# Optimization experiments

Hardware: AMD Instinct MI355X
Metric: run time of the kernel (lower is better)

Reference implementation:

```python
import jax, jax.numpy as jnp
import numpy as np

K = 1024
T = 16384
P = 2          # number of lags
N_STAGES = 2   # len(s_list)
EDGE_P = 0.005 # edge density -> avg degree ~5


def setup_inputs() -> dict:
    key = jax.random.key(0)
    kX, kA, ka, kb0, kb1 = jax.random.split(key, 5)
    X = jax.random.normal(kX, (K, T), dtype=jnp.float32)
    # sparse symmetric 0/1 adjacency, zero diagonal
    U = jax.random.uniform(kA, (K, K))
    Ab = (U < EDGE_P)
    Ab = (Ab | Ab.T) & ~jnp.eye(K, dtype=bool)
    A = Ab.astype(jnp.float32)
    alpha = jax.random.normal(ka, (P,), dtype=jnp.float32)
    beta0 = jax.random.normal(kb0, (P,), dtype=jnp.float32)
    beta1 = jax.random.normal(kb1, (P,), dtype=jnp.float32)
    return {"X": X, "A": A, "alpha": alpha, "beta0": beta0, "beta1": beta1}


def _stage_avg_matrices(A):
    """M[r] averages over nodes at shortest-path distance exactly r+1 (rows with
    no stage-r neighbors are all-zero, matching the `if neighbors:` guard)."""
    Ab = A > 0.5
    Af = Ab.astype(jnp.float32)
    reach_prev = jnp.eye(A.shape[0], dtype=bool)  # distance <= 0
    Ms = []
    for _ in range(N_STAGES):
        reach = reach_prev | ((reach_prev.astype(jnp.float32) @ Af) > 0.5)
        exact = reach & ~reach_prev                     # distance == r+1
        exact_f = exact.astype(jnp.float32)
        deg = exact_f.sum(axis=1, keepdims=True)        # (K, 1)
        M = exact_f / jnp.maximum(deg, 1.0)             # zero rows stay zero
        Ms.append(M)
        reach_prev = reach
    return Ms


def reference(X, A, alpha, beta0, beta1):
    K_, T_ = X.shape
    betas = [beta0, beta1]
    Ms = _stage_avg_matrices(A)
    # one dense aggregation per stage over ALL time steps, then slice lags
    MXs = [M @ X for M in Ms]                           # each (K, T)
    Y = jnp.zeros((K_, T_ - P), dtype=X.dtype)
    for lag in range(1, P + 1):
        sl = slice(P - lag, T_ - lag)
        Y = Y + alpha[lag - 1] * X[:, sl]
        for stage in range(N_STAGES):
            Y = Y + betas[stage][lag - 1] * MXs[stage][:, sl]
    return Y
```

## Files before the change

### kernel.cpp

```cpp
#include <hip/hip_runtime.h>

typedef float fx4 __attribute__((ext_vector_type(4)));
typedef short s16x8 __attribute__((ext_vector_type(8)));
typedef __bf16 bfx8 __attribute__((ext_vector_type(8)));

#define KN 1024
#define TT 16384
#define NOUT 16382
#define NKT 32

#define APK_OFF 67108864u

__device__ __forceinline__ unsigned short f2bf(float f) {
  return __builtin_bit_cast(unsigned short, (__bf16)f);
}

__device__ __forceinline__ void gll16(const void* g, void* l) {
  __builtin_amdgcn_global_load_lds(
      (const __attribute__((address_space(1))) void*)g,
      (__attribute__((address_space(3))) void*)l, 16, 0, 0);
}

__global__ __launch_bounds__(256) void k_masks(const float* __restrict__ A,
                                               unsigned* __restrict__ B1) {
  int k = blockIdx.x;
  int tid = threadIdx.x;
  int wv = tid >> 6, lane = tid & 63;
  for (int i = 0; i < 4; ++i) {
    int n = i * 256 + wv * 64 + lane;
    bool bit = (A[(size_t)k * KN + n] > 0.5f) && (n != k);
    unsigned long long m = __ballot(bit);
    if (lane == 0) {
      B1[k * 32 + i * 8 + wv * 2]     = (unsigned)m;
      B1[k * 32 + i * 8 + wv * 2 + 1] = (unsigned)(m >> 32);
    }
  }
}

__global__ __launch_bounds__(256) void k_weights(const unsigned* __restrict__ B1,
                                                 const float* __restrict__ alpha,
                                                 const float* __restrict__ beta0,
                                                 const float* __restrict__ beta1,
                                                 unsigned short* __restrict__ Wc) {
  __shared__ unsigned reach[32];
  __shared__ unsigned ex2[32];
  __shared__ unsigned short list[1056];
  __shared__ int nl;
  int k = blockIdx.x, tid = threadIdx.x;
  if (tid == 0) nl = 0;
  if (tid < 32) {
    unsigned r = B1[k * 32 + tid];
    if (tid == (k >> 5)) r |= 1u << (k & 31);
    reach[tid] = r;
    ex2[tid] = 0;
  }
  __syncthreads();
  for (int m = tid; m < KN; m += 256)
    if ((reach[m >> 5] >> (m & 31)) & 1) {
      int i = atomicAdd(&nl, 1);
      list[i] = (unsigned short)m;
    }
  __syncthreads();
  int n2 = nl;
  for (int i = 0; i < n2; ++i) {
    int m = list[i];
    if (tid < 32) ex2[tid] |= B1[m * 32 + tid];
  }
  __syncthreads();
  if (tid < 32) ex2[tid] &= ~reach[tid];
  __syncthreads();
  int d1 = 0, d2 = 0;
  for (int w = 0; w < 32; ++w) { d1 += __popc(reach[w]); d2 += __popc(ex2[w]); }
  d1 -= 1;
  float rd1 = 1.0f / fmaxf((float)d1, 1.0f);
  float rd2 = 1.0f / fmaxf((float)d2, 1.0f);
  float c00 = beta0[0] * rd1, c01 = beta0[1] * rd1;
  float c10 = beta1[0] * rd2, c11 = beta1[1] * rd2;
  float a0 = alpha[0], a1 = alpha[1];
  int mb = k >> 8, rloc = k & 255;
  for (int q = 0; q < 4; ++q) {
    int n = tid * 4 + q;
    bool in1 = (((reach[n >> 5] >> (n & 31)) & 1) != 0) && (n != k);
    bool in2 = ((ex2[n >> 5] >> (n & 31)) & 1) != 0;
    float v0 = (in1 ? c00 : 0.f) + (in2 ? c10 : 0.f) + (n == k ? a0 : 0.f);
    float v1 = (in1 ? c01 : 0.f) + (in2 ? c11 : 0.f) + (n == k ? a1 : 0.f);
    int kt = n >> 5, qk = (n >> 4) & 1, kb = (n >> 2) & 3, ii = (n & 3) * 2;
    size_t idx = ((((size_t)(mb * 32 + kt) * 2 + qk) * 4 + kb) * 256 + rloc) * 8 + ii;
    unsigned pair = (unsigned)f2bf(v0) | ((unsigned)f2bf(v1) << 16);
    *reinterpret_cast<unsigned*>(Wc + idx) = pair;
  }
}

__global__ __launch_bounds__(256) void k_pack_x2(const float* __restrict__ X,
                                                 unsigned short* __restrict__ Bpk) {
  int G = blockIdx.x * 256 + threadIdx.x;
  int col = G & 255;
  int kb  = (G >> 8) & 3;
  int qk  = (G >> 10) & 1;
  int kt  = (G >> 11) & 31;
  int jb  = G >> 16;
  int j   = jb * 256 + col;
  int mbase = kt * 32 + qk * 16 + kb * 4;
  unsigned v[4];
#pragma unroll
  for (int p = 0; p < 4; ++p) {
    int m = mbase + p;
    int j1 = j + 1;
    float f0 = (j1 < TT) ? X[(size_t)m * TT + j1] : 0.0f;
    float f1 = X[(size_t)m * TT + j];
    v[p] = (unsigned)f2bf(f0) | ((unsigned)f2bf(f1) << 16);
  }
  uint4 w; w.x = v[0]; w.y = v[1]; w.z = v[2]; w.w = v[3];
  *reinterpret_cast<uint4*>(Bpk + (size_t)G * 8) = w;
}

__global__ __launch_bounds__(512, 2) void k_gemm(const char* __restrict__ Apk,
                                                 const char* __restrict__ Bpk,
                                                 float* __restrict__ Y) {
  __shared__ char lds[131072];
  int bid = blockIdx.x;
  int swz = (bid & 7) * 32 + (bid >> 3);
  int jb = swz >> 2, mb = swz & 3;
  int tid = threadIdx.x;
  int lane = tid & 63, wv = tid >> 6;
  int wm = wv >> 2, wn = wv & 3;
  int kb = lane >> 4, ml = lane & 15;
  const char* Asrc = Apk + (size_t)mb * (NKT * 2 * 16384);
  const char* Bsrc = Bpk + (size_t)jb * (NKT * 2 * 16384);

  fx4 acc[2][4][4];
#pragma unroll
  for (int q = 0; q < 2; ++q)
#pragma unroll
    for (int a = 0; a < 4; ++a)
#pragma unroll
      for (int b = 0; b < 4; ++b) acc[q][a][b] = (fx4){0.f, 0.f, 0.f, 0.f};

  auto stage_half = [&](int tile, int isB, int qh) {
    char* dst = lds + (tile & 1) * 65536 + isB * 32768 + qh * 16384;
    const char* src = (isB ? Bsrc : Asrc) + ((size_t)(tile & (NKT - 1)) * 2 + qh) * 16384;
    gll16(src + tid * 16, dst + tid * 16);
    gll16(src + (size_t)(tid + 512) * 16, dst + (tid + 512) * 16);
  };

#define READ_A(dst, t, qk, qm)                                                      \
  do {                                                                              \
    const char* Ah_ = lds + ((t) & 1) * 65536 + (qk) * 16384;                       \
    _Pragma("unroll") for (int mf = 0; mf < 4; ++mf)                                \
      dst[mf] = *(const s16x8*)(Ah_ +                                               \
          (size_t)(kb * 256 + wm * 128 + (qm) * 64 + mf * 16 + ml) * 16);           \
  } while (0)
#define READ_B(dst, t, qk)                                                          \
  do {                                                                              \
    const char* Bh_ = lds + ((t) & 1) * 65536 + 32768 + (qk) * 16384;               \
    _Pragma("unroll") for (int nf = 0; nf < 4; ++nf)                                \
      dst[nf] = *(const s16x8*)(Bh_ +                                               \
          (size_t)(kb * 256 + wn * 64 + nf * 16 + ml) * 16);                        \
  } while (0)
#define MFMA16(acc_, a_, b_)                                                        \
  do {                                                                              \
    __builtin_amdgcn_s_setprio(1);                                                  \
    _Pragma("unroll") for (int mf = 0; mf < 4; ++mf)                                \
      _Pragma("unroll") for (int nf = 0; nf < 4; ++nf)                              \
        acc_[mf][nf] = __builtin_amdgcn_mfma_f32_16x16x32_bf16(                     \
            __builtin_bit_cast(bfx8, a_[mf]), __builtin_bit_cast(bfx8, b_[nf]),     \
            acc_[mf][nf], 0, 0, 0);                                                 \
    __builtin_amdgcn_s_setprio(0);                                                  \
  } while (0)

  s16x8 aA[4], aB[4], bA[4], bB[4];

  stage_half(0, 0, 0); stage_half(0, 1, 0);
  stage_half(0, 0, 1); stage_half(0, 1, 1);
  stage_half(1, 0, 0); stage_half(1, 1, 0);
  asm volatile("s_waitcnt vmcnt(4)" ::: "memory");
  __builtin_amdgcn_s_barrier();
  READ_A(aA, 0, 0, 0);
  READ_B(bA, 0, 0);

  for (int kt = 0; kt < NKT; ++kt) {
    READ_A(aB, kt, 0, 1);
    stage_half(kt + 1, 0, 1);
    MFMA16(acc[0], aA, bA);
    READ_A(aA, kt, 1, 0);
    READ_B(bB, kt, 1);
    stage_half(kt + 1, 1, 1);
    MFMA16(acc[1], aB, bA);
    asm volatile("s_waitcnt vmcnt(4)" ::: "memory");
    __builtin_amdgcn_s_barrier();
    READ_A(aB, kt, 1, 1);
    stage_half(kt + 2, 0, 0);
    MFMA16(acc[0], aA, bB);
    READ_A(aA, kt + 1, 0, 0);
    READ_B(bA, kt + 1, 0);
    stage_half(kt + 2, 1, 0);
    MFMA16(acc[1], aB, bB);
    asm volatile("s_waitcnt vmcnt(4)" ::: "memory");
    __builtin_amdgcn_s_barrier();
  }
  asm volatile("s_waitcnt vmcnt(0)" ::: "memory");

  int c0 = jb * 256 + wn * 64;
  int r0 = mb * 256 + wm * 128;
#pragma unroll
  for (int qm = 0; qm < 2; ++qm)
#pragma unroll
    for (int mf = 0; mf < 4; ++mf)
#pragma unroll
      for (int nf = 0; nf < 4; ++nf) {
        int c = c0 + nf * 16 + ml;
        if (c < NOUT) {
          int r = r0 + qm * 64 + mf * 16 + (lane >> 4) * 4;
#pragma unroll
          for (int i = 0; i < 4; ++i)
            Y[(size_t)(r + i) * NOUT + c] = acc[qm][mf][nf][i];
        }
      }
#undef READ_A
#undef READ_B
#undef MFMA16
}

extern "C" void kernel_launch(void* const* d_in, const int* in_sizes, int n_in,
                              void* d_out, int out_size, void* d_ws, size_t ws_size,
                              hipStream_t stream) {
  const float* X     = (const float*)d_in[0];
  const float* A     = (const float*)d_in[1];
  const float* alpha = (const float*)d_in[2];
  const float* beta0 = (const float*)d_in[3];
  const float* beta1 = (const float*)d_in[4];
  float* Y = (float*)d_out;
  char* ws = (char*)d_ws;
  char* Bpk = ws;
  char* Apk = ws + APK_OFF;
  unsigned* B1 = (unsigned*)ws;

  k_masks<<<dim3(1024), dim3(256), 0, stream>>>(A, B1);
  k_weights<<<dim3(1024), dim3(256), 0, stream>>>(B1, alpha, beta0, beta1,
                                                  (unsigned short*)Apk);
  k_pack_x2<<<dim3(16384), dim3(256), 0, stream>>>(X, (unsigned short*)Bpk);
  k_gemm<<<dim3(256), dim3(512), 0, stream>>>(Apk, Bpk, Y);
}
```

Measured before the change: 94.23 us.

## Switch GEMM to 32x32x16 bf16 MFMA with matching operand packing layout

Replaces the 16x16x32 MFMA tiling with 32x32x16 bf16 MFMA instructions, so each wave computes 4x2 fragments of 32x32 instead of 2x4x4 of 16x16. The packing kernels for both the weight matrix and the lagged X operand are rewritten to a new K-slice/octet layout that matches the 32x32 operand fragment format, and the LDS read and epilogue store indexing are updated to match. The larger MFMA reduces LDS fragment reads per FLOP and instruction issue overhead, at the cost of different register pressure and a strided epilogue write pattern.

```diff
diff --git a/kernel.cpp b/kernel.cpp
--- a/kernel.cpp
+++ b/kernel.cpp
@@ -1,6 +1,6 @@
 #include <hip/hip_runtime.h>
 
-typedef float fx4 __attribute__((ext_vector_type(4)));
+typedef float f32x16 __attribute__((ext_vector_type(16)));
 typedef short s16x8 __attribute__((ext_vector_type(8)));
 typedef __bf16 bfx8 __attribute__((ext_vector_type(8)));
 
@@ -84,8 +84,9 @@
     bool in2 = ((ex2[n >> 5] >> (n & 31)) & 1) != 0;
     float v0 = (in1 ? c00 : 0.f) + (in2 ? c10 : 0.f) + (n == k ? a0 : 0.f);
     float v1 = (in1 ? c01 : 0.f) + (in2 ? c11 : 0.f) + (n == k ? a1 : 0.f);
-    int kt = n >> 5, qk = (n >> 4) & 1, kb = (n >> 2) & 3, ii = (n & 3) * 2;
-    size_t idx = ((((size_t)(mb * 32 + kt) * 2 + qk) * 4 + kb) * 256 + rloc) * 8 + ii;
+    int kt = n >> 5, ks = (n >> 3) & 3, koct = (n >> 2) & 1, ii = (n & 3) * 2;
+    size_t idx = ((size_t)(mb * 32 + kt)) * 16384 + ks * 4096 + koct * 2048 +
+                 rloc * 8 + ii;
     unsigned pair = (unsigned)f2bf(v0) | ((unsigned)f2bf(v1) << 16);
     *reinterpret_cast<unsigned*>(Wc + idx) = pair;
   }
@@ -94,13 +95,13 @@
 __global__ __launch_bounds__(256) void k_pack_x2(const float* __restrict__ X,
                                                  unsigned short* __restrict__ Bpk) {
   int G = blockIdx.x * 256 + threadIdx.x;
-  int col = G & 255;
-  int kb  = (G >> 8) & 3;
-  int qk  = (G >> 10) & 1;
-  int kt  = (G >> 11) & 31;
-  int jb  = G >> 16;
-  int j   = jb * 256 + col;
-  int mbase = kt * 32 + qk * 16 + kb * 4;
+  int col  = G & 255;
+  int koct = (G >> 8) & 1;
+  int ks   = (G >> 9) & 3;
+  int kt   = (G >> 11) & 31;
+  int jb   = G >> 16;
+  int j    = jb * 256 + col;
+  int mbase = kt * 32 + ks * 8 + koct * 4;
   unsigned v[4];
 #pragma unroll
   for (int p = 0; p < 4; ++p) {
@@ -124,17 +125,19 @@
   int tid = threadIdx.x;
   int lane = tid & 63, wv = tid >> 6;
   int wm = wv >> 2, wn = wv & 3;
-  int kb = lane >> 4, ml = lane & 15;
-  const char* Asrc = Apk + (size_t)mb * (NKT * 2 * 16384);
-  const char* Bsrc = Bpk + (size_t)jb * (NKT * 2 * 16384);
-
-  fx4 acc[2][4][4];
-#pragma unroll
-  for (int q = 0; q < 2; ++q)
-#pragma unroll
-    for (int a = 0; a < 4; ++a)
-#pragma unroll
-      for (int b = 0; b < 4; ++b) acc[q][a][b] = (fx4){0.f, 0.f, 0.f, 0.f};
+  int l31 = lane & 31, loct = lane >> 5;
+  const char* Asrc = Apk + (size_t)mb * (NKT * 32768);
+  const char* Bsrc = Bpk + (size_t)jb * (NKT * 32768);
+  int aofs = loct * 4096 + (wm * 128 + l31) * 16;
+  int bofs = 32768 + loct * 4096 + (wn * 64 + l31) * 16;
+
+  f32x16 acc[4][2];
+#pragma unroll
+  for (int a = 0; a < 4; ++a)
+#pragma unroll
+    for (int b = 0; b < 2; ++b)
+#pragma unroll
+      for (int r = 0; r < 16; ++r) acc[a][b][r] = 0.f;
 
   auto stage_half = [&](int tile, int isB, int qh) {
     char* dst = lds + (tile & 1) * 65536 + isB * 32768 + qh * 16384;
@@ -143,82 +146,72 @@
     gll16(src + (size_t)(tid + 512) * 16, dst + (tid + 512) * 16);
   };
 
-#define READ_A(dst, t, qk, qm)                                                      \
+#define READ_F(ad, bd, t, ks)                                                       \
   do {                                                                              \
-    const char* Ah_ = lds + ((t) & 1) * 65536 + (qk) * 16384;                       \
+    const char* base_ = lds + ((t) & 1) * 65536 + (ks) * 8192;                      \
     _Pragma("unroll") for (int mf = 0; mf < 4; ++mf)                                \
-      dst[mf] = *(const s16x8*)(Ah_ +                                               \
-          (size_t)(kb * 256 + wm * 128 + (qm) * 64 + mf * 16 + ml) * 16);           \
+      ad[mf] = *(const s16x8*)(base_ + aofs + mf * 512);                            \
+    _Pragma("unroll") for (int nf = 0; nf < 2; ++nf)                                \
+      bd[nf] = *(const s16x8*)(base_ + bofs + nf * 512);                            \
   } while (0)
-#define READ_B(dst, t, qk)                                                          \
-  do {                                                                              \
-    const char* Bh_ = lds + ((t) & 1) * 65536 + 32768 + (qk) * 16384;               \
-    _Pragma("unroll") for (int nf = 0; nf < 4; ++nf)                                \
-      dst[nf] = *(const s16x8*)(Bh_ +                                               \
-          (size_t)(kb * 256 + wn * 64 + nf * 16 + ml) * 16);                        \
-  } while (0)
-#define MFMA16(acc_, a_, b_)                                                        \
+#define MFMA8(a_, b_)                                                               \
   do {                                                                              \
     __builtin_amdgcn_s_setprio(1);                                                  \
     _Pragma("unroll") for (int mf = 0; mf < 4; ++mf)                                \
-      _Pragma("unroll") for (int nf = 0; nf < 4; ++nf)                              \
-        acc_[mf][nf] = __builtin_amdgcn_mfma_f32_16x16x32_bf16(                     \
+      _Pragma("unroll") for (int nf = 0; nf < 2; ++nf)                              \
+        acc[mf][nf] = __builtin_amdgcn_mfma_f32_32x32x16_bf16(                      \
             __builtin_bit_cast(bfx8, a_[mf]), __builtin_bit_cast(bfx8, b_[nf]),     \
-            acc_[mf][nf], 0, 0, 0);                                                 \
+            acc[mf][nf], 0, 0, 0);                                                  \
     __builtin_amdgcn_s_setprio(0);                                                  \
   } while (0)
 
-  s16x8 aA[4], aB[4], bA[4], bB[4];
+  s16x8 aC[4], aN[4], bC[2], bN[2];
 
   stage_half(0, 0, 0); stage_half(0, 1, 0);
   stage_half(0, 0, 1); stage_half(0, 1, 1);
   stage_half(1, 0, 0); stage_half(1, 1, 0);
   asm volatile("s_waitcnt vmcnt(4)" ::: "memory");
   __builtin_amdgcn_s_barrier();
-  READ_A(aA, 0, 0, 0);
-  READ_B(bA, 0, 0);
+  READ_F(aC, bC, 0, 0);
 
   for (int kt = 0; kt < NKT; ++kt) {
-    READ_A(aB, kt, 0, 1);
+    READ_F(aN, bN, kt, 1);
     stage_half(kt + 1, 0, 1);
-    MFMA16(acc[0], aA, bA);
-    READ_A(aA, kt, 1, 0);
-    READ_B(bB, kt, 1);
+    MFMA8(aC, bC);
+    READ_F(aC, bC, kt, 2);
     stage_half(kt + 1, 1, 1);
-    MFMA16(acc[1], aB, bA);
+    MFMA8(aN, bN);
     asm volatile("s_waitcnt vmcnt(4)" ::: "memory");
     __builtin_amdgcn_s_barrier();
-    READ_A(aB, kt, 1, 1);
+    READ_F(aN, bN, kt, 3);
     stage_half(kt + 2, 0, 0);
-    MFMA16(acc[0], aA, bB);
-    READ_A(aA, kt + 1, 0, 0);
-    READ_B(bA, kt + 1, 0);
+    MFMA8(aC, bC);
+    READ_F(aC, bC, kt + 1, 0);
     stage_half(kt + 2, 1, 0);
-    MFMA16(acc[1], aB, bB);
+    MFMA8(aN, bN);
     asm volatile("s_waitcnt vmcnt(4)" ::: "memory");
     __builtin_amdgcn_s_barrier();
   }
   asm volatile("s_waitcnt vmcnt(0)" ::: "memory");
 
   int c0 = jb * 256 + wn * 64;
-  int r0 = mb * 256 + wm * 128;
-#pragma unroll
-  for (int qm = 0; qm < 2; ++qm)
-#pragma unroll
-    for (int mf = 0; mf < 4; ++mf)
-#pragma unroll
-      for (int nf = 0; nf < 4; ++nf) {
-        int c = c0 + nf * 16 + ml;
-        if (c < NOUT) {
-          int r = r0 + qm * 64 + mf * 16 + (lane >> 4) * 4;
-#pragma unroll
-          for (int i = 0; i < 4; ++i)
-            Y[(size_t)(r + i) * NOUT + c] = acc[qm][mf][nf][i];
+  int r0 = mb * 256 + wm * 128 + 4 * loct;
+#pragma unroll
+  for (int mf = 0; mf < 4; ++mf)
+#pragma unroll
+    for (int nf = 0; nf < 2; ++nf) {
+      int c = c0 + nf * 32 + l31;
+      if (c < NOUT) {
+        int rb = r0 + mf * 32;
+#pragma unroll
+        for (int reg = 0; reg < 16; ++reg) {
+          int r = rb + (reg & 3) + 8 * (reg >> 2);
+          Y[(size_t)r * NOUT + c] = acc[mf][nf][reg];
         }
       }
-#undef READ_A
-#undef READ_B
-#undef MFMA16
+    }
+#undef READ_F
+#undef MFMA8
 }
 
 extern "C" void kernel_launch(void* const* d_in, const int* in_sizes, int n_in,
```

After: 101.6 us. 1.08x slower.

## Fuse X bf16 packing into GEMM by loading fp32 X through registers

Applied to the files above, without the earlier changes.

Removes the separate k_pack_x2 kernel and its intermediate packed workspace. The GEMM now loads fp32 X directly into registers, converts it to lag-paired bf16 and writes it to LDS, pipelined with the async A staging. This drops one kernel launch and the write-then-reread of the packed B buffer. In exchange the GEMM issues many scalar strided fp32 loads per thread, which costs more registers and needs careful vmcnt accounting. Each 256-column X tile is also read by four M-blocks, and every thread reads two adjacent columns.

```diff
diff --git a/kernel.cpp b/kernel.cpp
--- a/kernel.cpp
+++ b/kernel.cpp
@@ -9,7 +9,7 @@
 #define NOUT 16382
 #define NKT 32
 
-#define APK_OFF 67108864u
+#define B1_OFF 4194304u
 
 __device__ __forceinline__ unsigned short f2bf(float f) {
   return __builtin_bit_cast(unsigned short, (__bf16)f);
@@ -91,31 +91,8 @@
   }
 }
 
-__global__ __launch_bounds__(256) void k_pack_x2(const float* __restrict__ X,
-                                                 unsigned short* __restrict__ Bpk) {
-  int G = blockIdx.x * 256 + threadIdx.x;
-  int col = G & 255;
-  int kb  = (G >> 8) & 3;
-  int qk  = (G >> 10) & 1;
-  int kt  = (G >> 11) & 31;
-  int jb  = G >> 16;
-  int j   = jb * 256 + col;
-  int mbase = kt * 32 + qk * 16 + kb * 4;
-  unsigned v[4];
-#pragma unroll
-  for (int p = 0; p < 4; ++p) {
-    int m = mbase + p;
-    int j1 = j + 1;
-    float f0 = (j1 < TT) ? X[(size_t)m * TT + j1] : 0.0f;
-    float f1 = X[(size_t)m * TT + j];
-    v[p] = (unsigned)f2bf(f0) | ((unsigned)f2bf(f1) << 16);
-  }
-  uint4 w; w.x = v[0]; w.y = v[1]; w.z = v[2]; w.w = v[3];
-  *reinterpret_cast<uint4*>(Bpk + (size_t)G * 8) = w;
-}
-
 __global__ __launch_bounds__(512, 2) void k_gemm(const char* __restrict__ Apk,
-                                                 const char* __restrict__ Bpk,
+                                                 const float* __restrict__ X,
                                                  float* __restrict__ Y) {
   __shared__ char lds[131072];
   int bid = blockIdx.x;
@@ -125,8 +102,13 @@
   int lane = tid & 63, wv = tid >> 6;
   int wm = wv >> 2, wn = wv & 3;
   int kb = lane >> 4, ml = lane & 15;
-  const char* Asrc = Apk + (size_t)mb * (NKT * 2 * 16384);
-  const char* Bsrc = Bpk + (size_t)jb * (NKT * 2 * 16384);
+  const char* Asrc = Apk + (size_t)mb * (NKT * 32768);
+
+  int col = tid & 255;
+  int kbq = tid >> 8;
+  int j = jb * 256 + col;
+  bool jlast = (j == TT - 1);
+  int jx = jlast ? (TT - 2) : j;
 
   fx4 acc[2][4][4];
 #pragma unroll
@@ -136,13 +118,38 @@
 #pragma unroll
       for (int b = 0; b < 4; ++b) acc[q][a][b] = (fx4){0.f, 0.f, 0.f, 0.f};
 
-  auto stage_half = [&](int tile, int isB, int qh) {
-    char* dst = lds + (tile & 1) * 65536 + isB * 32768 + qh * 16384;
-    const char* src = (isB ? Bsrc : Asrc) + ((size_t)(tile & (NKT - 1)) * 2 + qh) * 16384;
+  auto stage_A = [&](int tile, int qh) {
+    char* dst = lds + (tile & 1) * 65536 + qh * 16384;
+    const char* src = Asrc + ((size_t)(tile & (NKT - 1)) * 2 + qh) * 16384;
     gll16(src + tid * 16, dst + tid * 16);
     gll16(src + (size_t)(tid + 512) * 16, dst + (tid + 512) * 16);
   };
 
+#define BLOAD(ra, rb, t, qh)                                                        \
+  do {                                                                              \
+    int mq_ = ((t) & (NKT - 1)) * 32 + (qh) * 16 + kbq * 4;                         \
+    _Pragma("unroll") for (int p = 0; p < 4; ++p) {                                 \
+      const float* xp_ = X + (size_t)(mq_ + p) * TT + jx;                           \
+      ra[p] = xp_[0]; rb[p] = xp_[1];                                               \
+      const float* xq_ = X + (size_t)(mq_ + 8 + p) * TT + jx;                       \
+      ra[4 + p] = xq_[0]; rb[4 + p] = xq_[1];                                       \
+    }                                                                               \
+  } while (0)
+#define BWRITE(ra, rb, t, qh)                                                       \
+  do {                                                                              \
+    char* db_ = lds + ((t) & 1) * 65536 + 32768 + (qh) * 16384 + tid * 16;          \
+    uint4 w0_, w1_;                                                                 \
+    unsigned pr_[8];                                                                \
+    _Pragma("unroll") for (int p = 0; p < 8; ++p) {                                 \
+      float f1_ = jlast ? rb[p] : ra[p];                   \
+      float f0_ = jlast ? 0.f : rb[p];                     \
+      pr_[p] = (unsigned)f2bf(f0_) | ((unsigned)f2bf(f1_) << 16);                   \
+    }                                                                               \
+    w0_.x = pr_[0]; w0_.y = pr_[1]; w0_.z = pr_[2]; w0_.w = pr_[3];                 \
+    w1_.x = pr_[4]; w1_.y = pr_[5]; w1_.z = pr_[6]; w1_.w = pr_[7];                 \
+    *reinterpret_cast<uint4*>(db_) = w0_;                                           \
+    *reinterpret_cast<uint4*>(db_ + 8192) = w1_;                                    \
+  } while (0)
 #define READ_A(dst, t, qk, qm)                                                      \
   do {                                                                              \
     const char* Ah_ = lds + ((t) & 1) * 65536 + (qk) * 16384;                       \
@@ -169,33 +176,44 @@
   } while (0)
 
   s16x8 aA[4], aB[4], bA[4], bB[4];
-
-  stage_half(0, 0, 0); stage_half(0, 1, 0);
-  stage_half(0, 0, 1); stage_half(0, 1, 1);
-  stage_half(1, 0, 0); stage_half(1, 1, 0);
-  asm volatile("s_waitcnt vmcnt(4)" ::: "memory");
+  float ra0[8], rb0[8], ra1[8], rb1[8], ra[8], rb[8];
+
+  BLOAD(ra0, rb0, 0, 0); stage_A(0, 0);
+  BLOAD(ra1, rb1, 0, 1); stage_A(0, 1);
+  BLOAD(ra, rb, 1, 0);   stage_A(1, 0);
+  asm volatile("s_waitcnt vmcnt(38)" ::: "memory");
+  BWRITE(ra0, rb0, 0, 0);
+  asm volatile("s_waitcnt vmcnt(20)" ::: "memory");
+  BWRITE(ra1, rb1, 0, 1);
+  asm volatile("s_waitcnt vmcnt(2)" ::: "memory");
+  BWRITE(ra, rb, 1, 0);
+  asm volatile("s_waitcnt lgkmcnt(0)" ::: "memory");
   __builtin_amdgcn_s_barrier();
   READ_A(aA, 0, 0, 0);
   READ_B(bA, 0, 0);
 
   for (int kt = 0; kt < NKT; ++kt) {
     READ_A(aB, kt, 0, 1);
-    stage_half(kt + 1, 0, 1);
+    BLOAD(ra, rb, kt + 1, 1);
+    stage_A(kt + 1, 1);
     MFMA16(acc[0], aA, bA);
     READ_A(aA, kt, 1, 0);
     READ_B(bB, kt, 1);
-    stage_half(kt + 1, 1, 1);
     MFMA16(acc[1], aB, bA);
-    asm volatile("s_waitcnt vmcnt(4)" ::: "memory");
+    asm volatile("s_waitcnt vmcnt(2)" ::: "memory");
+    BWRITE(ra, rb, kt + 1, 1);
+    asm volatile("s_waitcnt lgkmcnt(0)" ::: "memory");
     __builtin_amdgcn_s_barrier();
     READ_A(aB, kt, 1, 1);
-    stage_half(kt + 2, 0, 0);
+    BLOAD(ra, rb, kt + 2, 0);
+    stage_A(kt + 2, 0);
     MFMA16(acc[0], aA, bB);
     READ_A(aA, kt + 1, 0, 0);
     READ_B(bA, kt + 1, 0);
-    stage_half(kt + 2, 1, 0);
     MFMA16(acc[1], aB, bB);
-    asm volatile("s_waitcnt vmcnt(4)" ::: "memory");
+    asm volatile("s_waitcnt vmcnt(2)" ::: "memory");
+    BWRITE(ra, rb, kt + 2, 0);
+    asm volatile("s_waitcnt lgkmcnt(0)" ::: "memory");
     __builtin_amdgcn_s_barrier();
   }
   asm volatile("s_waitcnt vmcnt(0)" ::: "memory");
@@ -216,6 +234,8 @@
             Y[(size_t)(r + i) * NOUT + c] = acc[qm][mf][nf][i];
         }
       }
+#undef BLOAD
+#undef BWRITE
 #undef READ_A
 #undef READ_B
 #undef MFMA16
@@ -231,13 +251,11 @@
   const float* beta1 = (const float*)d_in[4];
   float* Y = (float*)d_out;
   char* ws = (char*)d_ws;
-  char* Bpk = ws;
-  char* Apk = ws + APK_OFF;
-  unsigned* B1 = (unsigned*)ws;
+  char* Apk = ws;
+  unsigned* B1 = (unsigned*)(ws + B1_OFF);
 
   k_masks<<<dim3(1024), dim3(256), 0, stream>>>(A, B1);
   k_weights<<<dim3(1024), dim3(256), 0, stream>>>(B1, alpha, beta0, beta1,
                                                   (unsigned short*)Apk);
-  k_pack_x2<<<dim3(16384), dim3(256), 0, stream>>>(X, (unsigned short*)Bpk);
-  k_gemm<<<dim3(256), dim3(512), 0, stream>>>(Apk, Bpk, Y);
-}
+  k_gemm<<<dim3(256), dim3(512), 0, stream>>>(Apk, X, Y);
+}
```

Result: slower. 102.7 us (+9.0%).
